# Kernel tuning notes

Hardware: AMD Instinct MI355X
Metric: run time of the kernel (lower is better)

Reference implementation:

```python
import jax, jax.numpy as jnp
import numpy as np

D, NH, NL, NP, NLAYERS, DFF = 256, 8, 4, 4, 6, 1024
HD = D // NH
SHAPES = [(100, 100), (50, 50), (25, 25), (13, 13)]  # (H, W) per level
B = 4


def layernorm(x, w, b):
    m = x.mean(-1, keepdims=True)
    v = ((x - m) ** 2).mean(-1, keepdims=True)
    return (x - m) / jnp.sqrt(v + 1e-5) * w + b


def bilinear_sample(vl, loc, H, W):
    # vl: [B, H*W, NH, HD] level values; loc: [B, Lq, NH, NP, 2] normalized in [0,1]
    # matches F.grid_sample(bilinear, zeros padding, align_corners=False)
    bsz, Lq = loc.shape[0], loc.shape[1]
    px = loc[..., 0] * W - 0.5
    py = loc[..., 1] * H - 0.5
    x0 = jnp.floor(px); y0 = jnp.floor(py)
    wx1 = px - x0; wy1 = py - y0
    out = jnp.zeros((bsz, Lq, NH, NP, HD), vl.dtype)
    for xi, wx in ((x0, 1.0 - wx1), (x0 + 1.0, wx1)):
        for yi, wy in ((y0, 1.0 - wy1), (y0 + 1.0, wy1)):
            valid = (xi >= 0) & (xi < W) & (yi >= 0) & (yi < H)
            xc = jnp.clip(xi, 0, W - 1).astype(jnp.int32)
            yc = jnp.clip(yi, 0, H - 1).astype(jnp.int32)
            idx = yc * W + xc                                   # [B,Lq,NH,NP]
            idx2 = idx.transpose(0, 1, 3, 2).reshape(bsz, Lq * NP, NH, 1)
            g = jnp.take_along_axis(vl, idx2, axis=1)           # [B,Lq*NP,NH,HD]
            g = g.reshape(bsz, Lq, NP, NH, HD).transpose(0, 1, 3, 2, 4)
            w = (wx * wy * valid.astype(vl.dtype))[..., None]
            out = out + g * w
    return out


def get_reference_points(bsz):
    refs = []
    for (H, W) in SHAPES:
        ry = (jnp.arange(H, dtype=jnp.float32) + 0.5) / H
        rx = (jnp.arange(W, dtype=jnp.float32) + 0.5) / W
        gy, gx = jnp.meshgrid(ry, rx, indexing='ij')
        refs.append(jnp.stack([gx.reshape(-1), gy.reshape(-1)], -1))
    ref = jnp.concatenate(refs, 0)                              # [Len, 2]
    return jnp.broadcast_to(ref[None, :, None, :], (bsz, ref.shape[0], NL, 2))


def ms_deform_attn(query, src, ref, starts, so_w, so_b, aw_w, aw_b, vp_w, vp_b, op_w, op_b):
    bsz, Lq, _ = query.shape
    value = (src @ vp_w + vp_b).reshape(bsz, -1, NH, HD)
    offsets = (query @ so_w + so_b).reshape(bsz, Lq, NH, NL, NP, 2)
    aw = (query @ aw_w + aw_b).reshape(bsz, Lq, NH, NL * NP)
    aw = jax.nn.softmax(aw, -1).reshape(bsz, Lq, NH, NL, NP)
    normalizer = jnp.array([[W, H] for (H, W) in SHAPES], jnp.float32)  # x by W, y by H
    loc = ref[:, :, None, :, None, :] + offsets / normalizer[None, None, None, :, None, :]
    out = jnp.zeros((bsz, Lq, NH, HD), query.dtype)
    for l, (H, W) in enumerate(SHAPES):
        vl = value[:, starts[l]:starts[l] + H * W]
        sampled = bilinear_sample(vl, loc[:, :, :, l], H, W)    # [B,Lq,NH,NP,HD]
        out = out + jnp.einsum('blhp,blhpd->blhd', aw[:, :, :, l], sampled)
    return out.reshape(bsz, Lq, D) @ op_w + op_b


def setup_inputs():
    key = jax.random.key(0)
    ks = iter(jax.random.split(key, 64))
    d = {}
    for i, (H, W) in enumerate(SHAPES):
        d[f'src{i}'] = jax.random.normal(next(ks), (B, D, H, W), jnp.float32)
        d[f'pos{i}'] = jax.random.normal(next(ks), (B, D, H, W), jnp.float32)
    d['level_embed'] = jax.random.normal(next(ks), (NL, D), jnp.float32)
    d['so_w'] = jax.random.normal(next(ks), (NLAYERS, D, NH * NL * NP * 2), jnp.float32) * 0.005
    d['so_b'] = jax.random.normal(next(ks), (NLAYERS, NH * NL * NP * 2), jnp.float32) * 0.1
    d['aw_w'] = jax.random.normal(next(ks), (NLAYERS, D, NH * NL * NP), jnp.float32) * 0.02
    d['aw_b'] = jnp.zeros((NLAYERS, NH * NL * NP), jnp.float32)
    d['vp_w'] = jax.random.normal(next(ks), (NLAYERS, D, D), jnp.float32) * 0.02
    d['vp_b'] = jnp.zeros((NLAYERS, D), jnp.float32)
    d['op_w'] = jax.random.normal(next(ks), (NLAYERS, D, D), jnp.float32) * 0.02
    d['op_b'] = jnp.zeros((NLAYERS, D), jnp.float32)
    d['n1_w'] = jnp.ones((NLAYERS, D), jnp.float32)
    d['n1_b'] = jnp.zeros((NLAYERS, D), jnp.float32)
    d['f1_w'] = jax.random.normal(next(ks), (NLAYERS, D, DFF), jnp.float32) * 0.02
    d['f1_b'] = jnp.zeros((NLAYERS, DFF), jnp.float32)
    d['f2_w'] = jax.random.normal(next(ks), (NLAYERS, DFF, D), jnp.float32) * 0.02
    d['f2_b'] = jnp.zeros((NLAYERS, D), jnp.float32)
    d['n2_w'] = jnp.ones((NLAYERS, D), jnp.float32)
    d['n2_b'] = jnp.zeros((NLAYERS, D), jnp.float32)
    return d


def reference(src0, src1, src2, src3, pos0, pos1, pos2, pos3, level_embed,
              so_w, so_b, aw_w, aw_b, vp_w, vp_b, op_w, op_b,
              n1_w, n1_b, f1_w, f1_b, f2_w, f2_b, n2_w, n2_b):
    srcs = [src0, src1, src2, src3]
    poss = [pos0, pos1, pos2, pos3]
    bsz = src0.shape[0]
    src_flat, pos_flat, starts, off = [], [], [], 0
    for l, ((H, W), s, p) in enumerate(zip(SHAPES, srcs, poss)):
        starts.append(off); off += H * W
        src_flat.append(s.reshape(bsz, D, H * W).transpose(0, 2, 1))
        pos_flat.append(p.reshape(bsz, D, H * W).transpose(0, 2, 1) + level_embed[l][None, None, :])
    src = jnp.concatenate(src_flat, 1)                          # [B, Len, D]
    pos = jnp.concatenate(pos_flat, 1)
    ref = get_reference_points(bsz)
    for i in range(NLAYERS):
        q = src + pos
        attn = ms_deform_attn(q, src, ref, starts,
                              so_w[i], so_b[i], aw_w[i], aw_b[i],
                              vp_w[i], vp_b[i], op_w[i], op_b[i])
        src = layernorm(src + attn, n1_w[i], n1_b[i])
        h = jax.nn.relu(src @ f1_w[i] + f1_b[i]) @ f2_w[i] + f2_b[i]
        src = layernorm(src + h, n2_w[i], n2_b[i])
    level_start_index = jnp.array(starts, jnp.int64 if jax.config.jax_enable_x64 else jnp.int32)
    return src, level_start_index
```

## Files before the change

kernel.cpp:

```cpp
#include <hip/hip_runtime.h>

#define D 256
#define L_TOT 13294

typedef __attribute__((ext_vector_type(8))) __bf16 bf16x8;
typedef __attribute__((ext_vector_type(4))) float f32x4;
typedef __attribute__((ext_vector_type(2))) float f32x2;

__device__ __forceinline__ float bf2f(unsigned short u) {
    return __uint_as_float(((unsigned int)u) << 16);
}
__device__ __forceinline__ unsigned short f2bf(float f) {
    unsigned int u = __float_as_uint(f);
    u += 0x7FFFu + ((u >> 16) & 1u);
    return (unsigned short)(u >> 16);
}
__device__ __forceinline__ f32x2 bfpair(unsigned int d) {
    f32x2 r;
    r.x = __uint_as_float(d << 16);
    r.y = __uint_as_float(d & 0xFFFF0000u);
    return r;
}
__device__ __forceinline__ f32x2 fma2(f32x2 a, float w, f32x2 c) {
    return __builtin_elementwise_fma(a, (f32x2){w, w}, c);
}

__global__ void probe_k(const unsigned short* __restrict__ u, int n, int* __restrict__ flag)
{
    __shared__ int cnt;
    if (threadIdx.x == 0) cnt = 0;
    __syncthreads();
    int c = 0;
    for (int i = threadIdx.x; i < n; i += 256) {
        const int e = (u[i] >> 7) & 0xFF;
        if (e == 0 || (e >= 96 && e <= 150)) ++c;
    }
    atomicAdd(&cnt, c);
    __syncthreads();
    if (threadIdx.x == 0) *flag = (cnt * 10 > n * 9) ? 1 : 0;
}

__global__ __launch_bounds__(256) void convert_k(
    const void* __restrict__ src, unsigned short* __restrict__ dst, int n,
    const int* __restrict__ flag)
{
    const int i = blockIdx.x * 256 + threadIdx.x;
    if (i >= n) return;
    if (*flag) dst[i] = ((const unsigned short*)src)[i];
    else       dst[i] = f2bf(((const float*)src)[i]);
}

__global__ __launch_bounds__(256) void convt_k(
    const void* __restrict__ src, unsigned short* __restrict__ dst,
    int K, int N, int L, const int* __restrict__ flag)
{
    const long e = (long)blockIdx.x * 256 + threadIdx.x;
    const long tot = (long)L * K * N;
    if (e >= tot) return;
    const int per = K * N;
    const int li = (int)(e / per);
    const int r  = (int)(e - (long)li * per);
    const int n  = r / K;
    const int k  = r - n * K;
    const long s = (long)li * per + (long)k * N + n;
    dst[e] = (*flag) ? ((const unsigned short*)src)[s]
                     : f2bf(((const float*)src)[s]);
}

__global__ __launch_bounds__(256) void flatten_k(
    const void* __restrict__ s0, const void* __restrict__ s1,
    const void* __restrict__ s2, const void* __restrict__ s3,
    const int* __restrict__ flag, unsigned short* __restrict__ state)
{
    const long e = (long)blockIdx.x * 256 + threadIdx.x;
    const int d = (int)(e & 255);
    const long tok = e >> 8;
    const int b = (int)(tok / L_TOT);
    const int t = (int)(tok - (long)b * L_TOT);
    const void *sp;
    int hw, idx;
    if (t < 10000)      { sp = s0; hw = 10000; idx = t;          }
    else if (t < 12500) { sp = s1; hw = 2500;  idx = t - 10000;  }
    else if (t < 13125) { sp = s2; hw = 625;   idx = t - 12500;  }
    else                { sp = s3; hw = 169;   idx = t - 13125;  }
    const long a = ((long)b * D + d) * hw + idx;
    state[e] = (*flag) ? ((const unsigned short*)sp)[a]
                       : f2bf(((const float*)sp)[a]);
}

__global__ __launch_bounds__(256) void posconst_k(
    const void* __restrict__ p0, const void* __restrict__ p1,
    const void* __restrict__ p2, const void* __restrict__ p3,
    const unsigned short* __restrict__ lev, const int* __restrict__ flag,
    unsigned short* __restrict__ posc)
{
    const long e = (long)blockIdx.x * 256 + threadIdx.x;
    const int d = (int)(e & 255);
    const long tok = e >> 8;
    const int b = (int)(tok / L_TOT);
    const int t = (int)(tok - (long)b * L_TOT);
    const void *pp;
    int hw, idx, l;
    if (t < 10000)      { pp = p0; hw = 10000; idx = t;          l = 0; }
    else if (t < 12500) { pp = p1; hw = 2500;  idx = t - 10000;  l = 1; }
    else if (t < 13125) { pp = p2; hw = 625;   idx = t - 12500;  l = 2; }
    else                { pp = p3; hw = 169;   idx = t - 13125;  l = 3; }
    const long a = ((long)b * D + d) * hw + idx;
    const float pv = (*flag) ? bf2f(((const unsigned short*)pp)[a])
                             : ((const float*)pp)[a];
    posc[e] = f2bf(pv + bf2f(lev[l * D + d]));
}

__global__ __launch_bounds__(256) void addq_k(
    const unsigned short* __restrict__ x, const unsigned short* __restrict__ p,
    unsigned short* __restrict__ q, long n8)
{
    const long e = (long)blockIdx.x * 256 + threadIdx.x;
    if (e >= n8) return;
    const uint4 xv = ((const uint4*)x)[e];
    const uint4 pv = ((const uint4*)p)[e];
    uint4 o;
#define ADDPK(a, b) ({ const f32x2 fa = bfpair(a), fb = bfpair(b); \
        (unsigned int)f2bf(fb.x + fa.x) | ((unsigned int)f2bf(fb.y + fa.y) << 16); })
    o.x = ADDPK(xv.x, pv.x); o.y = ADDPK(xv.y, pv.y);
    o.z = ADDPK(xv.z, pv.z); o.w = ADDPK(xv.w, pv.w);
#undef ADDPK
    ((uint4*)q)[e] = o;
}

__global__ __launch_bounds__(256) void posflat_k(
    const void* __restrict__ p0, const void* __restrict__ p1,
    const void* __restrict__ p2, const void* __restrict__ p3,
    const unsigned short* __restrict__ lev, const int* __restrict__ flag,
    const unsigned short* __restrict__ x, unsigned short* __restrict__ q)
{
    const long e = (long)blockIdx.x * 256 + threadIdx.x;
    const int d = (int)(e & 255);
    const long tok = e >> 8;
    const int b = (int)(tok / L_TOT);
    const int t = (int)(tok - (long)b * L_TOT);
    const void *pp;
    int hw, idx, l;
    if (t < 10000)      { pp = p0; hw = 10000; idx = t;          l = 0; }
    else if (t < 12500) { pp = p1; hw = 2500;  idx = t - 10000;  l = 1; }
    else if (t < 13125) { pp = p2; hw = 625;   idx = t - 12500;  l = 2; }
    else                { pp = p3; hw = 169;   idx = t - 13125;  l = 3; }
    const long a = ((long)b * D + d) * hw + idx;
    const float pv = (*flag) ? bf2f(((const unsigned short*)pp)[a])
                             : ((const float*)pp)[a];
    q[e] = f2bf(pv + bf2f(lev[l * D + d]) + bf2f(x[e]));
}

template<bool RELU, bool RESID>
__device__ __forceinline__ void gemm_core(
    const unsigned short* __restrict__ A, int ldA,
    const unsigned short* __restrict__ Bt, int ldB,
    const unsigned short* __restrict__ bias,
    const unsigned short* resid,
    unsigned short* out, int ldO,
    long M, int K, int col0, long row0,
    unsigned short* As, unsigned short* Bs)
{
    const int tid = threadIdx.x;
    const int l  = tid & 63;
    const int w  = tid >> 6;
    const int wm = w >> 1, wn = w & 1;

    f32x4 acc[4][4];
#pragma unroll
    for (int i = 0; i < 4; ++i)
#pragma unroll
        for (int j = 0; j < 4; ++j) acc[i][j] = (f32x4){0.f, 0.f, 0.f, 0.f};

    const int sr = tid >> 3;
    const int sg = tid & 7;

    for (int k0 = 0; k0 < K; k0 += 64) {
#pragma unroll
        for (int i = 0; i < 4; ++i) {
            const int r = i * 32 + sr;
            long arow = row0 + r; if (arow >= M) arow = M - 1;
            const int ke = k0 + ((sg ^ (r & 7)) << 3);
            const unsigned short* ga = A  + arow * (long)ldA + ke;
            const unsigned short* gb = Bt + (long)(col0 + r) * ldB + ke;
            __builtin_amdgcn_global_load_lds(
                (const __attribute__((address_space(1))) void*)ga,
                (__attribute__((address_space(3))) void*)(As + i * 2048 + w * 512),
                16, 0, 0);
            __builtin_amdgcn_global_load_lds(
                (const __attribute__((address_space(1))) void*)gb,
                (__attribute__((address_space(3))) void*)(Bs + i * 2048 + w * 512),
                16, 0, 0);
        }
        __syncthreads();
#pragma unroll
        for (int ks = 0; ks < 2; ++ks) {
            const int cc  = ks * 4 + (l >> 4);
            const int swz = ((cc ^ (l & 7)) << 4);
            bf16x8 af[4], bfr[4];
#pragma unroll
            for (int mi = 0; mi < 4; ++mi) {
                const int ar = wm * 64 + mi * 16 + (l & 15);
                af[mi] = *(const bf16x8*)((const char*)As + ar * 128 + swz);
            }
#pragma unroll
            for (int ni = 0; ni < 4; ++ni) {
                const int br = wn * 64 + ni * 16 + (l & 15);
                bfr[ni] = *(const bf16x8*)((const char*)Bs + br * 128 + swz);
            }
#pragma unroll
            for (int mi = 0; mi < 4; ++mi)
#pragma unroll
                for (int ni = 0; ni < 4; ++ni)
                    acc[mi][ni] = __builtin_amdgcn_mfma_f32_16x16x32_bf16(
                        bfr[ni], af[mi], acc[mi][ni], 0, 0, 0);
        }
        __syncthreads();
    }

#pragma unroll
    for (int mi = 0; mi < 4; ++mi) {
        const long rr = row0 + wm * 64 + mi * 16 + (l & 15);
        if (rr >= M) continue;
#pragma unroll
        for (int ni = 0; ni < 4; ++ni) {
            const int col = col0 + wn * 64 + ni * 16 + (l >> 4) * 4;
            f32x4 v = acc[mi][ni];
            if (bias) {
                const ushort4 b4 = *(const ushort4*)(bias + col);
                v[0] += bf2f(b4.x); v[1] += bf2f(b4.y);
                v[2] += bf2f(b4.z); v[3] += bf2f(b4.w);
            }
            if (RELU) {
                v[0] = fmaxf(v[0], 0.f); v[1] = fmaxf(v[1], 0.f);
                v[2] = fmaxf(v[2], 0.f); v[3] = fmaxf(v[3], 0.f);
            }
            if (RESID) {
                const ushort4 r4 = *(const ushort4*)(resid + rr * (long)ldO + col);
                v[0] += bf2f(r4.x); v[1] += bf2f(r4.y);
                v[2] += bf2f(r4.z); v[3] += bf2f(r4.w);
            }
            ushort4 o;
            o.x = f2bf(v[0]); o.y = f2bf(v[1]); o.z = f2bf(v[2]); o.w = f2bf(v[3]);
            *(ushort4*)(out + rr * (long)ldO + col) = o;
        }
    }
}

template<bool RELU, bool RESID>
__global__ __launch_bounds__(256, 3) void mgemm_k(
    const unsigned short* __restrict__ A, int ldA,
    const unsigned short* __restrict__ Bt, int ldB,
    const unsigned short* __restrict__ bias,
    const unsigned short* resid,
    unsigned short* out, int ldOut,
    long M, int K)
{
    __shared__ unsigned short As[8192];
    __shared__ unsigned short Bs[8192];
    gemm_core<RELU, RESID>(A, ldA, Bt, ldB, bias, resid, out, ldOut,
                           M, K, blockIdx.x * 128, (long)blockIdx.y * 128, As, Bs);
}

__global__ __launch_bounds__(256, 3) void mgemm3_k(
    const unsigned short* __restrict__ state, const unsigned short* __restrict__ q,
    const unsigned short* __restrict__ Wv,  const unsigned short* __restrict__ bv,
    const unsigned short* __restrict__ Wso, const unsigned short* __restrict__ bso,
    const unsigned short* __restrict__ Waw, const unsigned short* __restrict__ baw,
    unsigned short* valo, unsigned short* offo, unsigned short* awo, long M)
{
    __shared__ unsigned short As[8192];
    __shared__ unsigned short Bs[8192];
    const int cx = blockIdx.x * 128;
    const long row0 = (long)blockIdx.y * 128;
    if (cx < 256)
        gemm_core<false, false>(state, D, Wv, D, bv, nullptr, valo, D,
                                M, D, cx, row0, As, Bs);
    else if (cx < 512)
        gemm_core<false, false>(q, D, Wso, D, bso, nullptr, offo, D,
                                M, D, cx - 256, row0, As, Bs);
    else
        gemm_core<false, false>(q, D, Waw, D, baw, nullptr, awo, 128,
                                M, D, 0, row0, As, Bs);
}

__global__ __launch_bounds__(256) void sample_k(
    const unsigned short* __restrict__ off, const unsigned short* __restrict__ aw,
    const unsigned short* __restrict__ val, unsigned short* __restrict__ attn)
{
    __shared__ __align__(16) int   cidx[128][4];
    __shared__ __align__(16) float cw[128][4];
    __shared__ float red[3][4][64];
    const long tok = blockIdx.x;
    const int tid = threadIdx.x;
    const int b = (int)(tok / L_TOT);
    const int t = (int)(tok - (long)b * L_TOT);

    if (tid < 128) {
        const int u = tid;
        const int lp = u & 15;
        const int mu = lp * 8 + (u >> 4);
        const int cswz = lp & 3;
        const float logit = bf2f(aw[tok * 128 + u]);
        float m = logit;
#pragma unroll
        for (int mk = 1; mk < 16; mk <<= 1) m = fmaxf(m, __shfl_xor(m, mk));
        const float e = expf(logit - m);
        float s = e;
#pragma unroll
        for (int mk = 1; mk < 16; mk <<= 1) s += __shfl_xor(s, mk);
        const float a = e / s;
        int st0, W0;
        if (t < 10000)      { st0 = 0;     W0 = 100; }
        else if (t < 12500) { st0 = 10000; W0 = 50;  }
        else if (t < 13125) { st0 = 12500; W0 = 25;  }
        else                { st0 = 13125; W0 = 13;  }
        const int i0 = t - st0;
        const int yy = i0 / W0;
        const int xx = i0 - yy * W0;
        const float gx = (xx + 0.5f) / (float)W0;
        const float gy = (yy + 0.5f) / (float)W0;
        const int lv = (u >> 2) & 3;
        const int Wv  = (lv == 0) ? 100 : (lv == 1) ? 50 : (lv == 2) ? 25 : 13;
        const int stl = (lv == 0) ? 0 : (lv == 1) ? 10000 : (lv == 2) ? 12500 : 13125;
        const unsigned int op = *(const unsigned int*)(off + tok * 256 + 2 * u);
        const float ox = bf2f((unsigned short)op);
        const float oy = bf2f((unsigned short)(op >> 16));
        const float px = (gx + ox / (float)Wv) * Wv - 0.5f;
        const float py = (gy + oy / (float)Wv) * Wv - 0.5f;
        const float fx = floorf(px), fy = floorf(py);
        const float wx1 = px - fx, wy1 = py - fy;
        const int x0 = (int)fx, y0 = (int)fy;
#pragma unroll
        for (int c = 0; c < 4; ++c) {
            const int xi = x0 + (c & 1);
            const int yi = y0 + (c >> 1);
            const float wgt = ((c & 1) ? wx1 : 1.f - wx1) * ((c >> 1) ? wy1 : 1.f - wy1);
            const bool ok = (xi >= 0) && (xi < Wv) && (yi >= 0) && (yi < Wv);
            cidx[mu][c ^ cswz] = ok ? ((stl + yi * Wv + xi) << 9) : 0;
            cw[mu][c ^ cswz]   = ok ? wgt * a : 0.f;
        }
    }
    __syncthreads();
    const int g = tid >> 6;
    const int l = tid & 63;
    const int h = l >> 3;
    const int q = l & 7;
    const char* vb = (const char*)val + ((long)b * L_TOT) * 512 + h * 64 + q * 8;
    f32x2 A01 = {0.f, 0.f}, A23 = {0.f, 0.f};
#pragma unroll
    for (int j = 0; j < 4; ++j) {
        const int mu = (j * 4 + g) * 8 + h;
        const int4   ci = *(const int4*)(&cidx[mu][0]);
        const float4 wv = *(const float4*)(&cw[mu][0]);
        const uint2 d0 = *(const uint2*)(vb + ci.x);
        const uint2 d1 = *(const uint2*)(vb + ci.y);
        const uint2 d2 = *(const uint2*)(vb + ci.z);
        const uint2 d3 = *(const uint2*)(vb + ci.w);
        A01 = fma2(bfpair(d0.x), wv.x, A01);  A23 = fma2(bfpair(d0.y), wv.x, A23);
        A01 = fma2(bfpair(d1.x), wv.y, A01);  A23 = fma2(bfpair(d1.y), wv.y, A23);
        A01 = fma2(bfpair(d2.x), wv.z, A01);  A23 = fma2(bfpair(d2.y), wv.z, A23);
        A01 = fma2(bfpair(d3.x), wv.w, A01);  A23 = fma2(bfpair(d3.y), wv.w, A23);
    }
    if (g) {
        red[g - 1][0][l] = A01.x; red[g - 1][1][l] = A01.y;
        red[g - 1][2][l] = A23.x; red[g - 1][3][l] = A23.y;
    }
    __syncthreads();
    if (g == 0) {
        float a0 = A01.x, a1 = A01.y, a2 = A23.x, a3 = A23.y;
#pragma unroll
        for (int p = 0; p < 3; ++p) {
            a0 += red[p][0][l]; a1 += red[p][1][l];
            a2 += red[p][2][l]; a3 += red[p][3][l];
        }
        ushort4 o;
        o.x = f2bf(a0); o.y = f2bf(a1); o.z = f2bf(a2); o.w = f2bf(a3);
        *(ushort4*)(attn + tok * 256 + h * 32 + q * 4) = o;
    }
}

template<bool QOUT>
__global__ __launch_bounds__(256) void ln_k(
    const unsigned short* __restrict__ y,
    const unsigned short* __restrict__ g, const unsigned short* __restrict__ bb,
    unsigned short* __restrict__ out,
    const unsigned short* __restrict__ posc, unsigned short* __restrict__ qout,
    long nt)
{
    const int wv = threadIdx.x >> 6;
    const int lane = threadIdx.x & 63;
    const long tok = (long)blockIdx.x * 4 + wv;
    if (tok >= nt) return;
    const ushort4 v4 = *(const ushort4*)(y + tok * D + lane * 4);
    const float v0 = bf2f(v4.x), v1 = bf2f(v4.y), v2 = bf2f(v4.z), v3 = bf2f(v4.w);
    float s = v0 + v1 + v2 + v3;
#pragma unroll
    for (int m = 1; m < 64; m <<= 1) s += __shfl_xor(s, m);
    const float mean = s * (1.f / D);
    const float d0 = v0 - mean, d1 = v1 - mean, d2 = v2 - mean, d3 = v3 - mean;
    float q = d0 * d0 + d1 * d1 + d2 * d2 + d3 * d3;
#pragma unroll
    for (int m = 1; m < 64; m <<= 1) q += __shfl_xor(q, m);
    const float rstd = rsqrtf(q * (1.f / D) + 1e-5f);
    const int c0 = lane * 4;
    ushort4 o;
    o.x = f2bf(d0 * rstd * bf2f(g[c0 + 0]) + bf2f(bb[c0 + 0]));
    o.y = f2bf(d1 * rstd * bf2f(g[c0 + 1]) + bf2f(bb[c0 + 1]));
    o.z = f2bf(d2 * rstd * bf2f(g[c0 + 2]) + bf2f(bb[c0 + 2]));
    o.w = f2bf(d3 * rstd * bf2f(g[c0 + 3]) + bf2f(bb[c0 + 3]));
    *(ushort4*)(out + tok * D + c0) = o;
    if (QOUT) {
        const ushort4 p4 = *(const ushort4*)(posc + tok * D + c0);
        ushort4 qo;
        qo.x = f2bf(bf2f(o.x) + bf2f(p4.x));
        qo.y = f2bf(bf2f(o.y) + bf2f(p4.y));
        qo.z = f2bf(bf2f(o.z) + bf2f(p4.z));
        qo.w = f2bf(bf2f(o.w) + bf2f(p4.w));
        *(ushort4*)(qout + tok * D + c0) = qo;
    }
}

__global__ __launch_bounds__(256) void finalize_k(
    const unsigned short* __restrict__ state, float* __restrict__ out, long osz)
{
    const long e = (long)blockIdx.x * 256 + threadIdx.x;
    const long n0 = osz - 4;
    if (e < n0) out[e] = bf2f(state[e]);
    if (e < 4) {
        const float st[4] = {0.f, 10000.f, 12500.f, 13125.f};
        out[n0 + e] = st[e];
    }
}

extern "C" void kernel_launch(void* const* d_in, const int* in_sizes, int n_in,
                              void* d_out, int out_size, void* d_ws, size_t ws_size,
                              hipStream_t stream)
{
    (void)n_in;
    const long osz = (long)out_size;
    const long nt = (osz - 4) / D;
    const int nlayers = in_sizes[9] / (D * D);
    const int dff = in_sizes[19] / (nlayers * D);

    char* ws = (char*)d_ws;
    int* flag = (int*)ws;  ws += 256;
    unsigned short* wc = (unsigned short*)ws;
    long off[25]; long acc_off = 0;
    for (int i = 8; i <= 24; ++i) { off[i] = acc_off; acc_off += in_sizes[i]; }
    ws += ((acc_off * 2 + 255) / 256) * 256;
    const size_t SZ_BF = (size_t)nt * D * 2;
    unsigned short* state     = (unsigned short*)ws;  ws += SZ_BF;
    unsigned short* val_b     = (unsigned short*)ws;  ws += SZ_BF;
    unsigned short* offy_b    = (unsigned short*)ws;  ws += SZ_BF;
    unsigned short* posattn_b = (unsigned short*)ws;  ws += SZ_BF;
    unsigned short* aw_b      = (unsigned short*)ws;  ws += (size_t)nt * 128 * 2;
    unsigned short* hbuf = val_b;

    const size_t used_base = (size_t)((char*)aw_b - (char*)d_ws) + (size_t)nt * 128 * 2;
    const bool have_posc = (ws_size >= used_base + SZ_BF);
    unsigned short* posc = (unsigned short*)((char*)d_ws + used_base);

    probe_k<<<1, 256, 0, stream>>>((const unsigned short*)d_in[8], in_sizes[8], flag);

    const int vecIdx[11] = {8, 10, 12, 14, 16, 17, 18, 20, 22, 23, 24};
    for (int j = 0; j < 11; ++j) {
        const int i = vecIdx[j];
        convert_k<<<(in_sizes[i] + 255) / 256, 256, 0, stream>>>(
            d_in[i], wc + off[i], in_sizes[i], flag);
    }
    const int matIdx[6] = {9, 11, 13, 15, 19, 21};
    const int matK[6]   = {D, D, D, D, D, dff};
    const int matN[6]   = {D, 128, D, D, dff, D};
    for (int j = 0; j < 6; ++j) {
        const int i = matIdx[j];
        convt_k<<<(in_sizes[i] + 255) / 256, 256, 0, stream>>>(
            d_in[i], wc + off[i], matK[j], matN[j], nlayers, flag);
    }

    flatten_k<<<(int)nt, 256, 0, stream>>>(
        d_in[0], d_in[2], d_in[4], d_in[6], flag, state);
    if (have_posc)
        posconst_k<<<(int)nt, 256, 0, stream>>>(
            d_in[1], d_in[3], d_in[5], d_in[7], wc + off[8], flag, posc);

    const int MB = (int)((nt + 127) / 128);
    const int LB = (int)((nt + 3) / 4);
    const long n8 = (long)nt * D / 8;
    const int AB = (int)((n8 + 255) / 256);
    const int dh = dff / 2;

    if (have_posc)
        addq_k<<<AB, 256, 0, stream>>>(state, posc, posattn_b, n8);

    for (int i = 0; i < nlayers; ++i) {
        if (!have_posc)
            posflat_k<<<(int)nt, 256, 0, stream>>>(
                d_in[1], d_in[3], d_in[5], d_in[7], wc + off[8], flag, state, posattn_b);
        mgemm3_k<<<dim3(5, MB), 256, 0, stream>>>(
            state, posattn_b,
            wc + off[13] + (long)i * D * D,   wc + off[14] + i * D,
            wc + off[9]  + (long)i * D * 256, wc + off[10] + i * 256,
            wc + off[11] + (long)i * D * 128, wc + off[12] + i * 128,
            val_b, offy_b, aw_b, nt);
        sample_k<<<(int)nt, 256, 0, stream>>>(offy_b, aw_b, val_b, posattn_b);
        mgemm_k<false, true><<<dim3(2, MB), 256, 0, stream>>>(
            posattn_b, D, wc + off[15] + (long)i * D * D, D, wc + off[16] + i * D,
            state, offy_b, D, nt, D);
        ln_k<false><<<LB, 256, 0, stream>>>(offy_b, wc + off[17] + i * D,
            wc + off[18] + i * D, state, nullptr, nullptr, nt);
        mgemm_k<true, false><<<dim3(dh / 128, MB), 256, 0, stream>>>(
            state, D, wc + off[19] + (long)i * D * dff, D, wc + off[20] + i * dff,
            nullptr, hbuf, dh, nt, D);
        mgemm_k<false, true><<<dim3(2, MB), 256, 0, stream>>>(
            hbuf, dh, wc + off[21] + (long)i * dff * D, dff, wc + off[22] + i * D,
            state, posattn_b, D, nt, dh);
        mgemm_k<true, false><<<dim3(dh / 128, MB), 256, 0, stream>>>(
            state, D, wc + off[19] + (long)i * D * dff + (long)dh * D, D,
            wc + off[20] + i * dff + dh, nullptr, hbuf, dh, nt, D);
        mgemm_k<false, true><<<dim3(2, MB), 256, 0, stream>>>(
            hbuf, dh, wc + off[21] + (long)i * dff * D + dh, dff, nullptr,
            posattn_b, posattn_b, D, nt, dh);
        if (have_posc && i + 1 < nlayers)
            ln_k<true><<<LB, 256, 0, stream>>>(posattn_b, wc + off[23] + i * D,
                wc + off[24] + i * D, state, posc, posattn_b, nt);
        else
            ln_k<false><<<LB, 256, 0, stream>>>(posattn_b, wc + off[23] + i * D,
                wc + off[24] + i * D, state, nullptr, nullptr, nt);
    }

    finalize_k<<<(int)((osz - 4 + 255) / 256), 256, 0, stream>>>(
        state, (float*)d_out, osz);
}
```

Measured before the change: 2.599 ms.

## Double-buffer GEMM LDS tiles with BK=32 and remap sample blocks per XCD

The GEMM core now stages K-tiles of 32 into two LDS buffers and issues the next tile's global-to-LDS loads before computing the current one. This uses a single barrier per iteration and overlaps memory latency with MFMA work. The LDS swizzle is rewritten for the 64-byte row pitch. Separately, the sampling kernel remaps block IDs so each XCD handles a contiguous range of tokens, aiming for better L2 locality on value gathers. The pipelined loop assumes the caller's LDS arrays are big enough for two buffers and that K is a multiple of 32.

```diff
diff --git a/kernel.cpp b/kernel.cpp
--- a/kernel.cpp
+++ b/kernel.cpp
@@ -172,51 +172,64 @@
 #pragma unroll
         for (int j = 0; j < 4; ++j) acc[i][j] = (f32x4){0.f, 0.f, 0.f, 0.f};
 
-    const int sr = tid >> 3;
-    const int sg = tid & 7;
-
-    for (int k0 = 0; k0 < K; k0 += 64) {
-#pragma unroll
-        for (int i = 0; i < 4; ++i) {
-            const int r = i * 32 + sr;
+    const int sr = tid >> 2;
+    const int sg = tid & 3;
+
+    auto stage = [&](int buf, int k0) {
+#pragma unroll
+        for (int i = 0; i < 2; ++i) {
+            const int r = i * 64 + sr;
             long arow = row0 + r; if (arow >= M) arow = M - 1;
-            const int ke = k0 + ((sg ^ (r & 7)) << 3);
+            const int s = (r & 3) ^ ((r >> 2) & 3);
+            const int ke = k0 + ((sg ^ s) << 3);
             const unsigned short* ga = A  + arow * (long)ldA + ke;
             const unsigned short* gb = Bt + (long)(col0 + r) * ldB + ke;
             __builtin_amdgcn_global_load_lds(
                 (const __attribute__((address_space(1))) void*)ga,
-                (__attribute__((address_space(3))) void*)(As + i * 2048 + w * 512),
+                (__attribute__((address_space(3))) void*)(As + buf * 4096 + i * 2048 + w * 512),
                 16, 0, 0);
             __builtin_amdgcn_global_load_lds(
                 (const __attribute__((address_space(1))) void*)gb,
-                (__attribute__((address_space(3))) void*)(Bs + i * 2048 + w * 512),
+                (__attribute__((address_space(3))) void*)(Bs + buf * 4096 + i * 2048 + w * 512),
                 16, 0, 0);
         }
+    };
+
+    auto compute = [&](int buf) {
+        const char* Ab = (const char*)As + buf * 8192;
+        const char* Bb = (const char*)Bs + buf * 8192;
+        const int cc = l >> 4;
+        bf16x8 af[4], bfr[4];
+#pragma unroll
+        for (int mi = 0; mi < 4; ++mi) {
+            const int ar = wm * 64 + mi * 16 + (l & 15);
+            const int p = cc ^ ((ar & 3) ^ ((ar >> 2) & 3));
+            af[mi] = *(const bf16x8*)(Ab + ar * 64 + (p << 4));
+        }
+#pragma unroll
+        for (int ni = 0; ni < 4; ++ni) {
+            const int br = wn * 64 + ni * 16 + (l & 15);
+            const int p = cc ^ ((br & 3) ^ ((br >> 2) & 3));
+            bfr[ni] = *(const bf16x8*)(Bb + br * 64 + (p << 4));
+        }
+#pragma unroll
+        for (int mi = 0; mi < 4; ++mi)
+#pragma unroll
+            for (int ni = 0; ni < 4; ++ni)
+                acc[mi][ni] = __builtin_amdgcn_mfma_f32_16x16x32_bf16(
+                    bfr[ni], af[mi], acc[mi][ni], 0, 0, 0);
+    };
+
+    stage(0, 0);
+    __syncthreads();
+    int cur = 0;
+    for (int k0 = 32; k0 < K; k0 += 32) {
+        stage(cur ^ 1, k0);
+        compute(cur);
         __syncthreads();
-#pragma unroll
-        for (int ks = 0; ks < 2; ++ks) {
-            const int cc  = ks * 4 + (l >> 4);
-            const int swz = ((cc ^ (l & 7)) << 4);
-            bf16x8 af[4], bfr[4];
-#pragma unroll
-            for (int mi = 0; mi < 4; ++mi) {
-                const int ar = wm * 64 + mi * 16 + (l & 15);
-                af[mi] = *(const bf16x8*)((const char*)As + ar * 128 + swz);
-            }
-#pragma unroll
-            for (int ni = 0; ni < 4; ++ni) {
-                const int br = wn * 64 + ni * 16 + (l & 15);
-                bfr[ni] = *(const bf16x8*)((const char*)Bs + br * 128 + swz);
-            }
-#pragma unroll
-            for (int mi = 0; mi < 4; ++mi)
-#pragma unroll
-                for (int ni = 0; ni < 4; ++ni)
-                    acc[mi][ni] = __builtin_amdgcn_mfma_f32_16x16x32_bf16(
-                        bfr[ni], af[mi], acc[mi][ni], 0, 0, 0);
-        }
-        __syncthreads();
-    }
+        cur ^= 1;
+    }
+    compute(cur);
 
 #pragma unroll
     for (int mi = 0; mi < 4; ++mi) {
@@ -291,7 +304,12 @@
     __shared__ __align__(16) int   cidx[128][4];
     __shared__ __align__(16) float cw[128][4];
     __shared__ float red[3][4][64];
-    const long tok = blockIdx.x;
+    const int nwg = (int)gridDim.x;
+    const int bid = (int)blockIdx.x;
+    const int qn = nwg >> 3, rn = nwg & 7;
+    const int xcd = bid & 7;
+    const int base = (xcd < rn) ? xcd * (qn + 1) : rn * (qn + 1) + (xcd - rn) * qn;
+    const long tok = (long)base + (bid >> 3);
     const int tid = threadIdx.x;
     const int b = (int)(tok / L_TOT);
     const int t = (int)(tok - (long)b * L_TOT);
```

New measurement: 2.736 ms. +5.3%, slower.
